# Kernel optimization log

Measured on AMD Instinct MI355X. Metric: run time of the kernel, lower is better.

Reference implementation:

```python
import jax, jax.numpy as jnp
import numpy as np

B, N, F, D, H, T = 32, 1024, 32, 64, 64, 4


def setup_inputs() -> dict:
    key = jax.random.key(0)
    ks = jax.random.split(key, 12)
    def w(k, shape):
        return 0.01 * jax.random.normal(k, shape, dtype=jnp.float32)
    z = lambda *s: jnp.zeros(s, jnp.float32)
    return {
        "xv": jax.random.normal(ks[0], (B, N, F), dtype=jnp.float32),
        "option": jax.random.uniform(ks[1], (B, 1), dtype=jnp.float32),
        "adj": jax.random.normal(ks[2], (N, N), dtype=jnp.float32),
        "mu1": w(ks[3], (F, D)),
        "W2": w(ks[4], (D, D)), "b2": z(D),
        "W3": w(ks[5], (D, D)), "b3": z(D),
        "W4": w(ks[6], (D, 1)), "b4": z(D),
        "Wq1": w(ks[7], (D, D)), "bq1": z(D),
        "Wq2": w(ks[8], (D, 1)), "bq2": z(D),
        "Wreg": w(ks[9], (H, 2 * D)), "breg": z(H),
        "Wq": w(ks[10], (1, H)), "bq": z(1),
    }


def reference(xv, option, adj, mu1, W2, b2, W3, b3, W4, b4,
              Wq1, bq1, Wq2, bq2, Wreg, breg, Wq, bq):
    # binary adjacency for message passing, raw weights for the mu_4 branch
    A = (adj > 0).astype(xv.dtype)                       # [N,N]
    mu_1 = jnp.maximum(xv @ mu1, 0.0)                    # [B,N,D]
    # mu_4: Linear(1,D) over every edge weight, clamp, sum over neighbors
    # (identical value every round t>=1, so computed once)
    mu4 = jnp.maximum(adj[..., None] * W4[:, 0] + b4, 0.0).sum(axis=1)[None]  # [1,N,D]
    mu3 = mu4 @ W3.T + b3                                # [1,N,D]
    mu = mu_1                                            # t = 0
    for _ in range(1, T):                                # t = 1..T-1
        mu_pool = jnp.einsum('nm,bmd->bnd', A, mu)       # neighbor aggregation
        mu2 = mu_pool @ W2.T + b2
        mu = jnp.maximum(mu_1 + mu2 + mu3, 0.0)
    mu_mean = jnp.maximum(mu.mean(axis=1, keepdims=True) @ Wq1.T + bq1, 0.0)  # [B,1,D]
    mu_aug = jnp.concatenate([mu, mu_mean], axis=1)      # [B,N+1,D]
    q2 = option.reshape(B, 1, 1) @ Wq2.T + bq2           # [B,1,D]
    q2 = jnp.broadcast_to(q2, (B, N + 1, D))
    q_ = jnp.concatenate([mu_aug, q2], axis=-1)          # [B,N+1,2D]
    qreg = jnp.maximum(q_ @ Wreg.T + breg, 0.0)          # [B,N+1,H]
    return qreg @ Wq.T + bq                              # [B,N+1,1]
```

## Files before the change

### kernel.cpp

```cpp
#include <hip/hip_runtime.h>
#include <hip/hip_bf16.h>

#define Bc 32
#define Nc 1024
#define Fc 32
#define Dc 64
#define Hc 64

typedef __bf16 bf16;
typedef __bf16 bf16x4 __attribute__((ext_vector_type(4)));
typedef __bf16 bf16x8 __attribute__((ext_vector_type(8)));
typedef float  f32x4  __attribute__((ext_vector_type(4)));

#define MS 72
#define LDS_RND_NONF 18432
#define LDS_RND_FIN  37376


__global__ void k_init(const float* __restrict__ adj, const float* __restrict__ W4,
                       const float* __restrict__ b4, const float* __restrict__ W3,
                       const float* __restrict__ b3, const float* __restrict__ b2,
                       const float* __restrict__ W2, const float* __restrict__ option,
                       const float* __restrict__ Wq2, const float* __restrict__ bq2,
                       const float* __restrict__ Wreg, const float* __restrict__ breg,
                       const float* __restrict__ xv, const float* __restrict__ mu1w,
                       bf16* __restrict__ Afrag, float* __restrict__ C3,
                       bf16* __restrict__ W2bf, float* __restrict__ c2base,
                       float* __restrict__ musum,
                       float* __restrict__ mu_1, bf16* __restrict__ Xfrag0) {
    const int id = blockIdx.x, t = threadIdx.x;
    __shared__ char smem[39424];
    if (id < 1024) {
        const int n = id;
        float* W3sT  = (float*)smem;
        float* red   = (float*)(smem + 16640);
        float* mu4_s = (float*)(smem + 17664);
        for (int i = t; i < 4096; i += 256)
            W3sT[(i & 63) * 65 + (i >> 6)] = W3[i];
        const float* arow = adj + (size_t)n * Nc;
        {
            const int m0 = t * 4;
            const float4 a = *(const float4*)&arow[m0];
            bf16x4 o;
            o[0] = (bf16)((a.x > 0.f) ? 1.f : 0.f);
            o[1] = (bf16)((a.y > 0.f) ? 1.f : 0.f);
            o[2] = (bf16)((a.z > 0.f) ? 1.f : 0.f);
            o[3] = (bf16)((a.w > 0.f) ? 1.f : 0.f);
            const int g = n >> 4, lm = n & 15;
            const int k0 = m0 >> 5, q = (m0 & 31) >> 3, j = m0 & 7;
            *(bf16x4*)&Afrag[(size_t)((g * 32 + k0) * 64 + lm + 16 * q) * 8 + j] = o;
        }
        const int e = t & 63, g = t >> 6;
        const float w4e = W4[e], b4e = b4[e];
        float acc = 0.f;
        const float4* arow4 = (const float4*)(arow + g * 256);
#pragma unroll 8
        for (int j = 0; j < 64; ++j) {
            const float4 av = arow4[j];
            acc += fmaxf(fmaf(av.x, w4e, b4e), 0.f);
            acc += fmaxf(fmaf(av.y, w4e, b4e), 0.f);
            acc += fmaxf(fmaf(av.z, w4e, b4e), 0.f);
            acc += fmaxf(fmaf(av.w, w4e, b4e), 0.f);
        }
        red[t] = acc;
        __syncthreads();
        if (g == 0) mu4_s[e] = red[e] + red[64 + e] + red[128 + e] + red[192 + e];
        __syncthreads();
        if (t < 64) {
            const int d = t;
            float a = b3[d] + b2[d];
#pragma unroll
            for (int ee = 0; ee < 64; ++ee) a = fmaf(mu4_s[ee], W3sT[ee * 65 + d], a);
            C3[n * 64 + d] = a;
        }
    } else if (id == 1024) {
        for (int j = t * 16; j < t * 16 + 16; ++j) W2bf[j] = (bf16)W2[j];
        for (int i = t; i < 2048; i += 256) musum[i] = 0.f;
        for (int i = t; i < 2048; i += 256) {
            const int b = i >> 6, h = i & 63;
            const float opt = option[b];
            float a = breg[h];
#pragma unroll
            for (int j = 0; j < 64; ++j)
                a = fmaf(fmaf(opt, Wq2[j], bq2[j]), Wreg[h * 128 + 64 + j], a);
            c2base[i] = a;
        }
    } else {
        const int idx = id - 1025, nb = idx & 15, b = idx >> 4;
        const int n0 = nb * 64;
        const int l = t & 63, wv = t >> 6, lm = l & 15, q = l >> 4;
        bf16* W2s = (bf16*)smem;
        bf16* xhi = (bf16*)(smem + 9216);
        bf16* xlo = (bf16*)(smem + 14336);
        bf16* whi = (bf16*)(smem + 19456);
        bf16* wlo = (bf16*)(smem + 24576);
        bf16* muS = (bf16*)(smem + 29696);
        {
            const int row = t >> 2, f0 = (t & 3) * 8;
            const float* src = &xv[((size_t)b * Nc + n0 + row) * Fc + f0];
            const float4 v0 = *(const float4*)src;
            const float4 v1 = *(const float4*)(src + 4);
            bf16x8 hi, lo;
            float vv[8] = {v0.x, v0.y, v0.z, v0.w, v1.x, v1.y, v1.z, v1.w};
#pragma unroll
            for (int j = 0; j < 8; ++j) { hi[j] = (bf16)vv[j]; lo[j] = (bf16)(vv[j] - (float)hi[j]); }
            *(bf16x8*)&xhi[row * 40 + f0] = hi;
            *(bf16x8*)&xlo[row * 40 + f0] = lo;
        }
        {
            const int d = t >> 2, f0 = (t & 3) * 8;
#pragma unroll
            for (int j = 0; j < 8; ++j) {
                const float v = mu1w[(f0 + j) * Dc + d];
                const bf16 hi = (bf16)v;
                whi[d * 40 + f0 + j] = hi;
                wlo[d * 40 + f0 + j] = (bf16)(v - (float)hi);
            }
        }
        {
            const int row = t >> 2, c0 = (t & 3) * 16;
            const float4 v0 = *(const float4*)&W2[row * 64 + c0];
            const float4 v1 = *(const float4*)&W2[row * 64 + c0 + 4];
            const float4 v2 = *(const float4*)&W2[row * 64 + c0 + 8];
            const float4 v3 = *(const float4*)&W2[row * 64 + c0 + 12];
            bf16x8 p0, p1;
            p0[0]=(bf16)v0.x; p0[1]=(bf16)v0.y; p0[2]=(bf16)v0.z; p0[3]=(bf16)v0.w;
            p0[4]=(bf16)v1.x; p0[5]=(bf16)v1.y; p0[6]=(bf16)v1.z; p0[7]=(bf16)v1.w;
            p1[0]=(bf16)v2.x; p1[1]=(bf16)v2.y; p1[2]=(bf16)v2.z; p1[3]=(bf16)v2.w;
            p1[4]=(bf16)v3.x; p1[5]=(bf16)v3.y; p1[6]=(bf16)v3.z; p1[7]=(bf16)v3.w;
            *(bf16x8*)&W2s[row * MS + c0] = p0;
            *(bf16x8*)&W2s[row * MS + c0 + 8] = p1;
        }
        __syncthreads();
        f32x4 acc[4];
#pragma unroll
        for (int ct = 0; ct < 4; ++ct)
#pragma unroll
            for (int r = 0; r < 4; ++r) acc[ct][r] = 0.f;
        {
            const bf16x8 aHi = *(const bf16x8*)&xhi[(wv * 16 + lm) * 40 + q * 8];
            const bf16x8 aLo = *(const bf16x8*)&xlo[(wv * 16 + lm) * 40 + q * 8];
#pragma unroll
            for (int ct = 0; ct < 4; ++ct) {
                const bf16x8 bHi = *(const bf16x8*)&whi[(ct * 16 + lm) * 40 + q * 8];
                const bf16x8 bLo = *(const bf16x8*)&wlo[(ct * 16 + lm) * 40 + q * 8];
                acc[ct] = __builtin_amdgcn_mfma_f32_16x16x32_bf16(aHi, bHi, acc[ct], 0, 0, 0);
                acc[ct] = __builtin_amdgcn_mfma_f32_16x16x32_bf16(aLo, bHi, acc[ct], 0, 0, 0);
                acc[ct] = __builtin_amdgcn_mfma_f32_16x16x32_bf16(aHi, bLo, acc[ct], 0, 0, 0);
            }
        }
#pragma unroll
        for (int ct = 0; ct < 4; ++ct) {
            const int col = ct * 16 + lm;
#pragma unroll
            for (int r = 0; r < 4; ++r) {
                const int row = wv * 16 + q * 4 + r;
                const float v = fmaxf(acc[ct][r], 0.f);
                mu_1[((size_t)b * Nc + n0 + row) * Dc + col] = v;
                muS[row * MS + col] = (bf16)v;
            }
        }
        __syncthreads();
        f32x4 xacc[4];
#pragma unroll
        for (int ct = 0; ct < 4; ++ct)
#pragma unroll
            for (int r = 0; r < 4; ++r) xacc[ct][r] = 0.f;
#pragma unroll
        for (int s = 0; s < 2; ++s) {
            bf16x8 a = *(const bf16x8*)&muS[(wv * 16 + lm) * MS + s * 32 + q * 8];
#pragma unroll
            for (int ct = 0; ct < 4; ++ct) {
                bf16x8 bv = *(const bf16x8*)&W2s[(ct * 16 + lm) * MS + s * 32 + q * 8];
                xacc[ct] = __builtin_amdgcn_mfma_f32_16x16x32_bf16(a, bv, xacc[ct], 0, 0, 0);
            }
        }
        const int k0 = nb * 2 + (wv >> 1);
        const int q_c = (wv & 1) * 2 + (q >> 1);
        const int j0 = (q & 1) * 4;
#pragma unroll
        for (int ct = 0; ct < 4; ++ct) {
            bf16x4 p;
#pragma unroll
            for (int r = 0; r < 4; ++r) p[r] = (bf16)xacc[ct][r];
            *(bf16x4*)&Xfrag0[(size_t)b * 65536
                              + (size_t)((ct * 32 + k0) * 64 + lm + 16 * q_c) * 8 + j0] = p;
        }
    }
}

template <bool FINAL>
__global__ __launch_bounds__(256, 2)
void k_round(const bf16* __restrict__ Afrag, const bf16* __restrict__ Xfr_in,
             const float* __restrict__ mu_1, const float* __restrict__ C3,
             const bf16* __restrict__ W2bf, bf16* __restrict__ Xfr_out,
             const float* __restrict__ Wreg, const float* __restrict__ c2base,
             const float* __restrict__ Wq, const float* __restrict__ bq,
             float* __restrict__ musum, float* __restrict__ out) {
    const int id = blockIdx.x, t = threadIdx.x;
    const int b  = ((id & 7) << 2) | ((id >> 3) & 3);
    const int nb = id >> 5;
    const int n0 = nb * 64;
    const int l = t & 63, wv = t >> 6, lm = l & 15, q = l >> 4;
    const int rh = wv & 1, ch = wv >> 1;
    extern __shared__ char smem[];
    bf16* muHi = (bf16*)smem;
    bf16* muLo = (bf16*)(smem + 9216);
    bf16* WHi  = (bf16*)(smem + (FINAL ? 18432 : 9216));
    bf16* WLo  = (bf16*)(smem + 27648);
    float* rpart = (float*)(smem + 36864);

    if (!FINAL) {
#pragma unroll
        for (int i = 0; i < 2; ++i) {
            int g = i * 256 + t, row = g >> 3, c = g & 7;
            *(bf16x8*)&WHi[row * MS + c * 8] = *(const bf16x8*)&W2bf[row * 64 + c * 8];
        }
    } else {
#pragma unroll
        for (int i = 0; i < 4; ++i) {
            int g = i * 1024 + t * 4, h = g >> 6, d = g & 63;
            const float4 w4 = *(const float4*)&Wreg[h * 128 + d];
            bf16x4 ohi, olo;
            ohi[0] = (bf16)w4.x; olo[0] = (bf16)(w4.x - (float)ohi[0]);
            ohi[1] = (bf16)w4.y; olo[1] = (bf16)(w4.y - (float)ohi[1]);
            ohi[2] = (bf16)w4.z; olo[2] = (bf16)(w4.z - (float)ohi[2]);
            ohi[3] = (bf16)w4.w; olo[3] = (bf16)(w4.w - (float)ohi[3]);
            *(bf16x4*)&WHi[h * MS + d] = ohi;
            *(bf16x4*)&WLo[h * MS + d] = olo;
        }
    }

    f32x4 acc[2][2];
#pragma unroll
    for (int rt = 0; rt < 2; ++rt)
#pragma unroll
        for (int ct = 0; ct < 2; ++ct)
#pragma unroll
            for (int r = 0; r < 4; ++r) acc[rt][ct][r] = 0.f;

    const int gA = nb * 4 + rh * 2;
    const bf16* pa0 = Afrag + (size_t)(gA + 0) * 32 * 512 + l * 8;
    const bf16* pa1 = Afrag + (size_t)(gA + 1) * 32 * 512 + l * 8;
    const bf16* px0 = Xfr_in + (size_t)b * 65536 + (size_t)(ch * 2 + 0) * 32 * 512 + l * 8;
    const bf16* px1 = Xfr_in + (size_t)b * 65536 + (size_t)(ch * 2 + 1) * 32 * 512 + l * 8;
#pragma unroll 4
    for (int k0 = 0; k0 < 32; ++k0) {
        const int o = k0 * 512;
        bf16x8 a0 = *(const bf16x8*)&pa0[o];
        bf16x8 a1 = *(const bf16x8*)&pa1[o];
        bf16x8 x0 = *(const bf16x8*)&px0[o];
        bf16x8 x1 = *(const bf16x8*)&px1[o];
        acc[0][0] = __builtin_amdgcn_mfma_f32_16x16x32_bf16(a0, x0, acc[0][0], 0, 0, 0);
        acc[0][1] = __builtin_amdgcn_mfma_f32_16x16x32_bf16(a0, x1, acc[0][1], 0, 0, 0);
        acc[1][0] = __builtin_amdgcn_mfma_f32_16x16x32_bf16(a1, x0, acc[1][0], 0, 0, 0);
        acc[1][1] = __builtin_amdgcn_mfma_f32_16x16x32_bf16(a1, x1, acc[1][1], 0, 0, 0);
    }

    float vals[2][2][4];
#pragma unroll
    for (int rt = 0; rt < 2; ++rt)
#pragma unroll
        for (int ct = 0; ct < 2; ++ct) {
            const int col = ch * 32 + ct * 16 + lm;
#pragma unroll
            for (int r = 0; r < 4; ++r) {
                const int n = n0 + rh * 32 + rt * 16 + q * 4 + r;
                float v = mu_1[((size_t)b * Nc + n) * Dc + col] + acc[rt][ct][r]
                        + C3[n * 64 + col];
                vals[rt][ct][r] = fmaxf(v, 0.f);
            }
        }

#pragma unroll
    for (int rt = 0; rt < 2; ++rt)
#pragma unroll
        for (int ct = 0; ct < 2; ++ct) {
            const int col = ch * 32 + ct * 16 + lm;
#pragma unroll
            for (int r = 0; r < 4; ++r) {
                const int row = rh * 32 + rt * 16 + q * 4 + r;
                const float v = vals[rt][ct][r];
                const bf16 hi = (bf16)v;
                muHi[row * MS + col] = hi;
                if (FINAL) muLo[row * MS + col] = (bf16)(v - (float)hi);
            }
        }
    if (FINAL) {
#pragma unroll
        for (int ct = 0; ct < 2; ++ct) {
            float s = 0.f;
#pragma unroll
            for (int rt = 0; rt < 2; ++rt)
#pragma unroll
                for (int r = 0; r < 4; ++r) s += vals[rt][ct][r];
            s += __shfl_xor(s, 16);
            s += __shfl_xor(s, 32);
            if (q == 0) atomicAdd(&musum[b * 64 + ch * 32 + ct * 16 + lm], s);
        }
    }
    __syncthreads();

    f32x4 xacc[2][2];
#pragma unroll
    for (int rt = 0; rt < 2; ++rt)
#pragma unroll
        for (int ct = 0; ct < 2; ++ct)
#pragma unroll
            for (int r = 0; r < 4; ++r) xacc[rt][ct][r] = 0.f;

    if (!FINAL) {
#pragma unroll
        for (int s = 0; s < 2; ++s) {
            bf16x8 aM[2], bW[2];
#pragma unroll
            for (int rt = 0; rt < 2; ++rt)
                aM[rt] = *(const bf16x8*)&muHi[(rh * 32 + rt * 16 + lm) * MS + s * 32 + q * 8];
#pragma unroll
            for (int ct = 0; ct < 2; ++ct)
                bW[ct] = *(const bf16x8*)&WHi[(ch * 32 + ct * 16 + lm) * MS + s * 32 + q * 8];
#pragma unroll
            for (int rt = 0; rt < 2; ++rt)
#pragma unroll
                for (int ct = 0; ct < 2; ++ct)
                    xacc[rt][ct] = __builtin_amdgcn_mfma_f32_16x16x32_bf16(aM[rt], bW[ct],
                                                                           xacc[rt][ct], 0, 0, 0);
        }
        const int k0 = nb * 2 + rh;
        const int q_c0 = (q >> 1), j0 = (q & 1) * 4;
#pragma unroll
        for (int rt = 0; rt < 2; ++rt)
#pragma unroll
            for (int ct = 0; ct < 2; ++ct) {
                bf16x4 p;
#pragma unroll
                for (int r = 0; r < 4; ++r) p[r] = (bf16)xacc[rt][ct][r];
                *(bf16x4*)&Xfr_out[(size_t)b * 65536
                    + (size_t)(((ch * 2 + ct) * 32 + k0) * 64 + lm + 16 * (rt * 2 + q_c0)) * 8
                    + j0] = p;
            }
    } else {
#pragma unroll
        for (int s = 0; s < 2; ++s) {
            bf16x8 aH[2], aL[2], bH[2], bL[2];
#pragma unroll
            for (int rt = 0; rt < 2; ++rt) {
                const int ao = (rh * 32 + rt * 16 + lm) * MS + s * 32 + q * 8;
                aH[rt] = *(const bf16x8*)&muHi[ao];
                aL[rt] = *(const bf16x8*)&muLo[ao];
            }
#pragma unroll
            for (int ct = 0; ct < 2; ++ct) {
                const int bo = (ch * 32 + ct * 16 + lm) * MS + s * 32 + q * 8;
                bH[ct] = *(const bf16x8*)&WHi[bo];
                bL[ct] = *(const bf16x8*)&WLo[bo];
            }
#pragma unroll
            for (int rt = 0; rt < 2; ++rt)
#pragma unroll
                for (int ct = 0; ct < 2; ++ct) {
                    xacc[rt][ct] = __builtin_amdgcn_mfma_f32_16x16x32_bf16(aH[rt], bH[ct],
                                                                           xacc[rt][ct], 0, 0, 0);
                    xacc[rt][ct] = __builtin_amdgcn_mfma_f32_16x16x32_bf16(aL[rt], bH[ct],
                                                                           xacc[rt][ct], 0, 0, 0);
                    xacc[rt][ct] = __builtin_amdgcn_mfma_f32_16x16x32_bf16(aH[rt], bL[ct],
                                                                           xacc[rt][ct], 0, 0, 0);
                }
        }
        const float bq0 = bq[0];
        float rowsum[2][4] = {{0.f, 0.f, 0.f, 0.f}, {0.f, 0.f, 0.f, 0.f}};
#pragma unroll
        for (int ct = 0; ct < 2; ++ct) {
            const int h = ch * 32 + ct * 16 + lm;
            const float c2 = c2base[b * 64 + h];
            const float wqh = Wq[h];
#pragma unroll
            for (int rt = 0; rt < 2; ++rt)
#pragma unroll
                for (int r = 0; r < 4; ++r)
                    rowsum[rt][r] += fmaxf(xacc[rt][ct][r] + c2, 0.f) * wqh;
        }
#pragma unroll
        for (int rt = 0; rt < 2; ++rt)
#pragma unroll
            for (int r = 0; r < 4; ++r) {
                float v = rowsum[rt][r];
                v += __shfl_xor(v, 1);
                v += __shfl_xor(v, 2);
                v += __shfl_xor(v, 4);
                v += __shfl_xor(v, 8);
                if (lm == 0) rpart[ch * 64 + rh * 32 + rt * 16 + q * 4 + r] = v;
            }
        __syncthreads();
        if (t < 64)
            out[(size_t)b * (Nc + 1) + n0 + t] = rpart[t] + rpart[64 + t] + bq0;
    }
}

__global__ void k_tail(const float* __restrict__ musum, const float* __restrict__ Wq1,
                       const float* __restrict__ bq1, const float* __restrict__ Wreg,
                       const float* __restrict__ c2base, const float* __restrict__ Wq,
                       const float* __restrict__ bq, float* __restrict__ out) {
    const int b = blockIdx.x, l = threadIdx.x;
    __shared__ float mean_s[64];
    __shared__ float mp[64];
    mean_s[l] = musum[b * 64 + l] * (1.f / Nc);
    __syncthreads();
    float a = bq1[l];
#pragma unroll
    for (int e = 0; e < 64; ++e) a = fmaf(mean_s[e], Wq1[l * 64 + e], a);
    mp[l] = fmaxf(a, 0.f);
    __syncthreads();
    float h = c2base[b * 64 + l];
#pragma unroll
    for (int d = 0; d < 64; ++d) h = fmaf(mp[d], Wreg[l * 128 + d], h);
    float v = fmaxf(h, 0.f) * Wq[l];
#pragma unroll
    for (int off = 32; off; off >>= 1) v += __shfl_down(v, off);
    if (l == 0) out[(size_t)b * (Nc + 1) + Nc] = v + bq[0];
}

extern "C" void kernel_launch(void* const* d_in, const int* in_sizes, int n_in,
                              void* d_out, int out_size, void* d_ws, size_t ws_size,
                              hipStream_t stream) {
    const float* xv     = (const float*)d_in[0];
    const float* option = (const float*)d_in[1];
    const float* adj    = (const float*)d_in[2];
    const float* mu1w   = (const float*)d_in[3];
    const float* W2     = (const float*)d_in[4];
    const float* b2     = (const float*)d_in[5];
    const float* W3     = (const float*)d_in[6];
    const float* b3     = (const float*)d_in[7];
    const float* W4     = (const float*)d_in[8];
    const float* b4     = (const float*)d_in[9];
    const float* Wq1    = (const float*)d_in[10];
    const float* bq1    = (const float*)d_in[11];
    const float* Wq2    = (const float*)d_in[12];
    const float* bq2    = (const float*)d_in[13];
    const float* Wreg   = (const float*)d_in[14];
    const float* breg   = (const float*)d_in[15];
    const float* Wq     = (const float*)d_in[16];
    const float* bq     = (const float*)d_in[17];
    float* out = (float*)d_out;

    float* ws = (float*)d_ws;
    const size_t MU = (size_t)Bc * Nc * Dc;
    float* mu_1     = ws;
    float* C3       = ws + MU;
    float* c2base   = C3 + 65536;
    float* musum    = c2base + 2048;
    bf16*  Afrag    = (bf16*)(musum + 2048);
    bf16*  W2bf     = Afrag + (size_t)Nc * Nc;
    bf16*  Xf0      = W2bf + 4096;
    bf16*  Xf1      = Xf0 + MU;

    k_init<<<1537, 256, 0, stream>>>(adj, W4, b4, W3, b3, b2, W2, option, Wq2, bq2,
                                     Wreg, breg, xv, mu1w,
                                     Afrag, C3, W2bf, c2base, musum, mu_1, Xf0);
    k_round<false><<<512, 256, LDS_RND_NONF, stream>>>(
        Afrag, Xf0, mu_1, C3, W2bf, Xf1,
        nullptr, nullptr, nullptr, nullptr, nullptr, nullptr);
    k_round<false><<<512, 256, LDS_RND_NONF, stream>>>(
        Afrag, Xf1, mu_1, C3, W2bf, Xf0,
        nullptr, nullptr, nullptr, nullptr, nullptr, nullptr);
    k_round<true><<<512, 256, LDS_RND_FIN, stream>>>(
        Afrag, Xf0, mu_1, C3, nullptr, nullptr,
        Wreg, c2base, Wq, bq, musum, out);
    k_tail<<<Bc, 64, 0, stream>>>(musum, Wq1, bq1, Wreg, c2base, Wq, bq, out);
}
```

Baseline: 153.9 us.

## Split K across waves in round kernels with LDS partial-sum reduction

Each wave now computes the full 64x64 aggregation tile over a quarter of the K dimension using a 4x4 MFMA accumulator grid, instead of a quarter of the tile over full K. This doubles fragment reuse per load, halving global/L2 load traffic for the adjacency and feature fragments. Partials are summed through a padded fp32 LDS buffer with extra barriers, raising LDS use and accumulator register pressure.

```diff
diff --git a/kernel.cpp b/kernel.cpp
--- a/kernel.cpp
+++ b/kernel.cpp
@@ -13,8 +13,8 @@
 typedef float  f32x4  __attribute__((ext_vector_type(4)));
 
 #define MS 72
-#define LDS_RND_NONF 18432
-#define LDS_RND_FIN  37376
+#define PS 68
+#define LDS_RND 44032
 
 
 __global__ void k_init(const float* __restrict__ adj, const float* __restrict__ W4,
@@ -204,11 +204,12 @@
     const int l = t & 63, wv = t >> 6, lm = l & 15, q = l >> 4;
     const int rh = wv & 1, ch = wv >> 1;
     extern __shared__ char smem[];
-    bf16* muHi = (bf16*)smem;
-    bf16* muLo = (bf16*)(smem + 9216);
-    bf16* WHi  = (bf16*)(smem + (FINAL ? 18432 : 9216));
-    bf16* WLo  = (bf16*)(smem + 27648);
-    float* rpart = (float*)(smem + 36864);
+    float* part = (float*)smem;
+    bf16* WHi   = (bf16*)(smem + 34816);
+    bf16* muHi  = (bf16*)smem;
+    bf16* muLo  = (bf16*)(smem + 9216);
+    bf16* WLo   = (bf16*)(smem + 18432);
+    float* rpart = (float*)(smem + 27648);
 
     if (!FINAL) {
 #pragma unroll
@@ -216,7 +217,127 @@
             int g = i * 256 + t, row = g >> 3, c = g & 7;
             *(bf16x8*)&WHi[row * MS + c * 8] = *(const bf16x8*)&W2bf[row * 64 + c * 8];
         }
-    } else {
+    }
+
+    f32x4 acc[4][4];
+#pragma unroll
+    for (int rt = 0; rt < 4; ++rt)
+#pragma unroll
+        for (int ct = 0; ct < 4; ++ct)
+#pragma unroll
+            for (int r = 0; r < 4; ++r) acc[rt][ct][r] = 0.f;
+
+    const bf16* pa[4];
+    const bf16* px[4];
+#pragma unroll
+    for (int g = 0; g < 4; ++g) {
+        pa[g] = Afrag + (size_t)(nb * 4 + g) * 16384 + wv * 4096 + l * 8;
+        px[g] = Xfr_in + (size_t)b * 65536 + (size_t)g * 16384 + wv * 4096 + l * 8;
+    }
+#pragma unroll 2
+    for (int k = 0; k < 8; ++k) {
+        const int o = k * 512;
+        bf16x8 a0 = *(const bf16x8*)&pa[0][o];
+        bf16x8 a1 = *(const bf16x8*)&pa[1][o];
+        bf16x8 a2 = *(const bf16x8*)&pa[2][o];
+        bf16x8 a3 = *(const bf16x8*)&pa[3][o];
+        bf16x8 x0 = *(const bf16x8*)&px[0][o];
+        bf16x8 x1 = *(const bf16x8*)&px[1][o];
+        bf16x8 x2 = *(const bf16x8*)&px[2][o];
+        bf16x8 x3 = *(const bf16x8*)&px[3][o];
+        acc[0][0] = __builtin_amdgcn_mfma_f32_16x16x32_bf16(a0, x0, acc[0][0], 0, 0, 0);
+        acc[0][1] = __builtin_amdgcn_mfma_f32_16x16x32_bf16(a0, x1, acc[0][1], 0, 0, 0);
+        acc[0][2] = __builtin_amdgcn_mfma_f32_16x16x32_bf16(a0, x2, acc[0][2], 0, 0, 0);
+        acc[0][3] = __builtin_amdgcn_mfma_f32_16x16x32_bf16(a0, x3, acc[0][3], 0, 0, 0);
+        acc[1][0] = __builtin_amdgcn_mfma_f32_16x16x32_bf16(a1, x0, acc[1][0], 0, 0, 0);
+        acc[1][1] = __builtin_amdgcn_mfma_f32_16x16x32_bf16(a1, x1, acc[1][1], 0, 0, 0);
+        acc[1][2] = __builtin_amdgcn_mfma_f32_16x16x32_bf16(a1, x2, acc[1][2], 0, 0, 0);
+        acc[1][3] = __builtin_amdgcn_mfma_f32_16x16x32_bf16(a1, x3, acc[1][3], 0, 0, 0);
+        acc[2][0] = __builtin_amdgcn_mfma_f32_16x16x32_bf16(a2, x0, acc[2][0], 0, 0, 0);
+        acc[2][1] = __builtin_amdgcn_mfma_f32_16x16x32_bf16(a2, x1, acc[2][1], 0, 0, 0);
+        acc[2][2] = __builtin_amdgcn_mfma_f32_16x16x32_bf16(a2, x2, acc[2][2], 0, 0, 0);
+        acc[2][3] = __builtin_amdgcn_mfma_f32_16x16x32_bf16(a2, x3, acc[2][3], 0, 0, 0);
+        acc[3][0] = __builtin_amdgcn_mfma_f32_16x16x32_bf16(a3, x0, acc[3][0], 0, 0, 0);
+        acc[3][1] = __builtin_amdgcn_mfma_f32_16x16x32_bf16(a3, x1, acc[3][1], 0, 0, 0);
+        acc[3][2] = __builtin_amdgcn_mfma_f32_16x16x32_bf16(a3, x2, acc[3][2], 0, 0, 0);
+        acc[3][3] = __builtin_amdgcn_mfma_f32_16x16x32_bf16(a3, x3, acc[3][3], 0, 0, 0);
+    }
+
+    if (wv < 2) {
+#pragma unroll
+        for (int rt = 0; rt < 4; ++rt)
+#pragma unroll
+            for (int ct = 0; ct < 4; ++ct)
+                *(f32x4*)&part[(wv * 64 + ct * 16 + lm) * PS + rt * 16 + q * 4] = acc[rt][ct];
+    }
+    __syncthreads();
+    if (wv >= 2) {
+#pragma unroll
+        for (int rt = 0; rt < 4; ++rt)
+#pragma unroll
+            for (int ct = 0; ct < 4; ++ct) {
+                float* p = &part[((wv - 2) * 64 + ct * 16 + lm) * PS + rt * 16 + q * 4];
+                f32x4 v = *(const f32x4*)p;
+                *(f32x4*)p = v + acc[rt][ct];
+            }
+    }
+    __syncthreads();
+    f32x4 psum[2][2];
+#pragma unroll
+    for (int rt = 0; rt < 2; ++rt)
+#pragma unroll
+        for (int ct = 0; ct < 2; ++ct) {
+            const int col = ch * 32 + ct * 16 + lm;
+            const int row = rh * 32 + rt * 16 + q * 4;
+            f32x4 s0 = *(const f32x4*)&part[col * PS + row];
+            f32x4 s1 = *(const f32x4*)&part[(64 + col) * PS + row];
+            psum[rt][ct] = s0 + s1;
+        }
+
+    float vals[2][2][4];
+#pragma unroll
+    for (int rt = 0; rt < 2; ++rt)
+#pragma unroll
+        for (int ct = 0; ct < 2; ++ct) {
+            const int col = ch * 32 + ct * 16 + lm;
+#pragma unroll
+            for (int r = 0; r < 4; ++r) {
+                const int n = n0 + rh * 32 + rt * 16 + q * 4 + r;
+                float v = mu_1[((size_t)b * Nc + n) * Dc + col] + psum[rt][ct][r]
+                        + C3[n * 64 + col];
+                vals[rt][ct][r] = fmaxf(v, 0.f);
+            }
+        }
+    if (FINAL) {
+#pragma unroll
+        for (int ct = 0; ct < 2; ++ct) {
+            float s = 0.f;
+#pragma unroll
+            for (int rt = 0; rt < 2; ++rt)
+#pragma unroll
+                for (int r = 0; r < 4; ++r) s += vals[rt][ct][r];
+            s += __shfl_xor(s, 16);
+            s += __shfl_xor(s, 32);
+            if (q == 0) atomicAdd(&musum[b * 64 + ch * 32 + ct * 16 + lm], s);
+        }
+    }
+    __syncthreads();
+
+#pragma unroll
+    for (int rt = 0; rt < 2; ++rt)
+#pragma unroll
+        for (int ct = 0; ct < 2; ++ct) {
+            const int col = ch * 32 + ct * 16 + lm;
+#pragma unroll
+            for (int r = 0; r < 4; ++r) {
+                const int row = rh * 32 + rt * 16 + q * 4 + r;
+                const float v = vals[rt][ct][r];
+                const bf16 hi = (bf16)v;
+                muHi[row * MS + col] = hi;
+                if (FINAL) muLo[row * MS + col] = (bf16)(v - (float)hi);
+            }
+        }
+    if (FINAL) {
 #pragma unroll
         for (int i = 0; i < 4; ++i) {
             int g = i * 1024 + t * 4, h = g >> 6, d = g & 63;
@@ -228,75 +349,6 @@
             ohi[3] = (bf16)w4.w; olo[3] = (bf16)(w4.w - (float)ohi[3]);
             *(bf16x4*)&WHi[h * MS + d] = ohi;
             *(bf16x4*)&WLo[h * MS + d] = olo;
-        }
-    }
-
-    f32x4 acc[2][2];
-#pragma unroll
-    for (int rt = 0; rt < 2; ++rt)
-#pragma unroll
-        for (int ct = 0; ct < 2; ++ct)
-#pragma unroll
-            for (int r = 0; r < 4; ++r) acc[rt][ct][r] = 0.f;
-
-    const int gA = nb * 4 + rh * 2;
-    const bf16* pa0 = Afrag + (size_t)(gA + 0) * 32 * 512 + l * 8;
-    const bf16* pa1 = Afrag + (size_t)(gA + 1) * 32 * 512 + l * 8;
-    const bf16* px0 = Xfr_in + (size_t)b * 65536 + (size_t)(ch * 2 + 0) * 32 * 512 + l * 8;
-    const bf16* px1 = Xfr_in + (size_t)b * 65536 + (size_t)(ch * 2 + 1) * 32 * 512 + l * 8;
-#pragma unroll 4
-    for (int k0 = 0; k0 < 32; ++k0) {
-        const int o = k0 * 512;
-        bf16x8 a0 = *(const bf16x8*)&pa0[o];
-        bf16x8 a1 = *(const bf16x8*)&pa1[o];
-        bf16x8 x0 = *(const bf16x8*)&px0[o];
-        bf16x8 x1 = *(const bf16x8*)&px1[o];
-        acc[0][0] = __builtin_amdgcn_mfma_f32_16x16x32_bf16(a0, x0, acc[0][0], 0, 0, 0);
-        acc[0][1] = __builtin_amdgcn_mfma_f32_16x16x32_bf16(a0, x1, acc[0][1], 0, 0, 0);
-        acc[1][0] = __builtin_amdgcn_mfma_f32_16x16x32_bf16(a1, x0, acc[1][0], 0, 0, 0);
-        acc[1][1] = __builtin_amdgcn_mfma_f32_16x16x32_bf16(a1, x1, acc[1][1], 0, 0, 0);
-    }
-
-    float vals[2][2][4];
-#pragma unroll
-    for (int rt = 0; rt < 2; ++rt)
-#pragma unroll
-        for (int ct = 0; ct < 2; ++ct) {
-            const int col = ch * 32 + ct * 16 + lm;
-#pragma unroll
-            for (int r = 0; r < 4; ++r) {
-                const int n = n0 + rh * 32 + rt * 16 + q * 4 + r;
-                float v = mu_1[((size_t)b * Nc + n) * Dc + col] + acc[rt][ct][r]
-                        + C3[n * 64 + col];
-                vals[rt][ct][r] = fmaxf(v, 0.f);
-            }
-        }
-
-#pragma unroll
-    for (int rt = 0; rt < 2; ++rt)
-#pragma unroll
-        for (int ct = 0; ct < 2; ++ct) {
-            const int col = ch * 32 + ct * 16 + lm;
-#pragma unroll
-            for (int r = 0; r < 4; ++r) {
-                const int row = rh * 32 + rt * 16 + q * 4 + r;
-                const float v = vals[rt][ct][r];
-                const bf16 hi = (bf16)v;
-                muHi[row * MS + col] = hi;
-                if (FINAL) muLo[row * MS + col] = (bf16)(v - (float)hi);
-            }
-        }
-    if (FINAL) {
-#pragma unroll
-        for (int ct = 0; ct < 2; ++ct) {
-            float s = 0.f;
-#pragma unroll
-            for (int rt = 0; rt < 2; ++rt)
-#pragma unroll
-                for (int r = 0; r < 4; ++r) s += vals[rt][ct][r];
-            s += __shfl_xor(s, 16);
-            s += __shfl_xor(s, 32);
-            if (q == 0) atomicAdd(&musum[b * 64 + ch * 32 + ct * 16 + lm], s);
         }
     }
     __syncthreads();
@@ -457,13 +509,13 @@
     k_init<<<1537, 256, 0, stream>>>(adj, W4, b4, W3, b3, b2, W2, option, Wq2, bq2,
                                      Wreg, breg, xv, mu1w,
                                      Afrag, C3, W2bf, c2base, musum, mu_1, Xf0);
-    k_round<false><<<512, 256, LDS_RND_NONF, stream>>>(
+    k_round<false><<<512, 256, LDS_RND, stream>>>(
         Afrag, Xf0, mu_1, C3, W2bf, Xf1,
         nullptr, nullptr, nullptr, nullptr, nullptr, nullptr);
-    k_round<false><<<512, 256, LDS_RND_NONF, stream>>>(
+    k_round<false><<<512, 256, LDS_RND, stream>>>(
         Afrag, Xf1, mu_1, C3, W2bf, Xf0,
         nullptr, nullptr, nullptr, nullptr, nullptr, nullptr);
-    k_round<true><<<512, 256, LDS_RND_FIN, stream>>>(
+    k_round<true><<<512, 256, LDS_RND, stream>>>(
         Afrag, Xf0, mu_1, C3, nullptr, nullptr,
         Wreg, c2base, Wq, bq, musum, out);
     k_tail<<<Bc, 64, 0, stream>>>(musum, Wq1, bq1, Wreg, c2base, Wq, bq, out);
```

Result: faster. 146.4 us, median of 2 (-4.9%).
